# Optimization experiments

Measured on AMD Instinct MI355X. Metric: run time of the kernel, lower is better.

Reference implementation:

```python
import jax, jax.numpy as jnp
import numpy as np

B, S, H = 2, 2048, 2048
NK, NV, DK, DV = 16, 32, 128, 128
K_CONV = 4
EPS = 1e-6
KEY_DIM = NK * DK          # 2048
VALUE_DIM = NV * DV        # 4096
CONV_DIM = 2 * KEY_DIM + VALUE_DIM  # 8192
R = NV // NK               # GQA repeat factor


def setup_inputs() -> dict:
    key = jax.random.key(0)
    ks = jax.random.split(key, 9)
    s = lambda d: 1.0 / np.sqrt(d)
    x = jax.random.normal(ks[0], (B, S, H), jnp.float32)
    W_qkvz = jax.random.normal(ks[1], (H, 2 * KEY_DIM + 2 * VALUE_DIM), jnp.float32) * s(H)
    W_ba = jax.random.normal(ks[2], (H, 2 * NV), jnp.float32) * s(H)
    conv_w = jax.random.normal(ks[3], (CONV_DIM, K_CONV), jnp.float32) * s(K_CONV)
    dt_bias = jnp.ones((NV,), jnp.float32)
    A_log = jnp.log(jax.random.uniform(ks[4], (NV,), jnp.float32, 1e-3, 16.0))
    norm_w = jnp.ones((DV,), jnp.float32)
    W_out = jax.random.normal(ks[5], (VALUE_DIM, H), jnp.float32) * s(VALUE_DIM)
    return {"x": x, "W_qkvz": W_qkvz, "W_ba": W_ba, "conv_w": conv_w,
            "dt_bias": dt_bias, "A_log": A_log, "norm_w": norm_w, "W_out": W_out}


def _rms_norm(x, eps=EPS):
    return x * jax.lax.rsqrt(jnp.mean(jnp.square(x), -1, keepdims=True) + eps)


def _forward(x, W_qkvz, W_ba, conv_w, dt_bias, A_log, norm_w, W_out):
    b_, s_ = x.shape[:2]
    # in projections (mlx split-INDEX semantics)
    qkvz = (x @ W_qkvz).reshape(b_, s_, NK, 2 * DK + 2 * R * DV)
    q, k, v, z = jnp.split(qkvz, [DK, 2 * DK, 2 * DK + R * DV], axis=-1)
    v = v.reshape(b_, s_, NV, DV)
    z = z.reshape(b_, s_, NV, DV)
    ba = (x @ W_ba).reshape(b_, s_, NK, 2 * R)
    b_gate, a_gate = jnp.split(ba, [R], axis=-1)
    b_gate = b_gate.reshape(b_, s_, NV)
    a_gate = a_gate.reshape(b_, s_, NV)

    # causal depthwise conv over [q,k,v] channels, zero initial conv state
    mixed = jnp.concatenate([q.reshape(b_, s_, -1), k.reshape(b_, s_, -1),
                             v.reshape(b_, s_, -1)], axis=-1)  # [B,S,CONV_DIM]
    xc = jnp.pad(mixed, ((0, 0), (K_CONV - 1, 0), (0, 0))).transpose(0, 2, 1)  # [B,C,S+K-1]
    conv = jax.lax.conv_general_dilated(
        xc, conv_w[:, None, :], window_strides=(1,), padding='VALID',
        dimension_numbers=('NCH', 'OIH', 'NCH'), feature_group_count=CONV_DIM)
    conv = jax.nn.silu(conv).transpose(0, 2, 1)  # [B,S,CONV_DIM]
    q, k, v = jnp.split(conv, [KEY_DIM, 2 * KEY_DIM], axis=-1)
    q = q.reshape(b_, s_, NK, DK)
    k = k.reshape(b_, s_, NK, DK)
    v = v.reshape(b_, s_, NV, DV)

    inv_scale = DK ** -0.5
    q = (inv_scale ** 2) * _rms_norm(q)
    k = inv_scale * _rms_norm(k)
    # GQA: repeat k/q heads to match value heads
    q = jnp.repeat(q, R, axis=2)  # [B,S,NV,DK]
    k = jnp.repeat(k, R, axis=2)

    beta = jax.nn.sigmoid(b_gate)                                # [B,S,NV]
    g = -jnp.exp(A_log) * jax.nn.softplus(a_gate + dt_bias)      # [B,S,NV] (log-decay)

    # gated delta-rule recurrence, scan over time
    def step(Sst, inp):
        q_t, k_t, v_t, g_t, beta_t = inp   # [B,NV,DK], [B,NV,DV], [B,NV]
        Sst = Sst * jnp.exp(g_t)[..., None, None]
        kv = jnp.einsum('bhk,bhkv->bhv', k_t, Sst)
        delta = (v_t - kv) * beta_t[..., None]
        Sst = Sst + k_t[..., None] * delta[:, :, None, :]
        o = jnp.einsum('bhk,bhkv->bhv', q_t, Sst)
        return Sst, o

    S0 = jnp.zeros((b_, NV, DK, DV), x.dtype)
    xs = (q.transpose(1, 0, 2, 3), k.transpose(1, 0, 2, 3), v.transpose(1, 0, 2, 3),
          g.transpose(1, 0, 2), beta.transpose(1, 0, 2))
    _, out = jax.lax.scan(step, S0, xs)
    out = out.transpose(1, 0, 2, 3)  # [B,S,NV,DV]

    # gated RMSNorm (precise swiglu)
    xn = _rms_norm(out) * norm_w
    gated = jax.nn.silu(z.astype(jnp.float32)) * xn.astype(jnp.float32)
    gated = gated.astype(x.dtype)
    return gated.reshape(b_, s_, VALUE_DIM) @ W_out


def reference(x, W_qkvz, W_ba, conv_w, dt_bias, A_log, norm_w, W_out):
    return _forward(x, W_qkvz, W_ba, conv_w, dt_bias, A_log, norm_w, W_out)
```

## Files before the change

### kernel.cpp

```cpp
#include <hip/hip_runtime.h>
#include <stdint.h>

#define B_    2
#define SEQ   2048
#define HID   2048
#define NK_   16
#define NV_   32
#define DK_   128
#define DV_   128
#define NQKVZ 12288
#define CONVD 8192
#define MTOT  (B_*SEQ)
#define CCH   16
#define T0TOK 1216
#define HTOK2 832
#define RLDSZ 110592

typedef unsigned short ushort_t;
typedef __bf16 bf16x8 __attribute__((ext_vector_type(8)));
typedef float  f32x4  __attribute__((ext_vector_type(4)));
typedef unsigned short us4 __attribute__((ext_vector_type(4)));

__device__ __forceinline__ ushort_t f2bf(float f){
  union { float f; unsigned u; } v; v.f = f;
  unsigned r = v.u + 0x7FFFu + ((v.u >> 16) & 1u);
  return (ushort_t)(r >> 16);
}
__device__ __forceinline__ float bf2f(ushort_t u){
  union { unsigned u; float f; } v; v.u = ((unsigned)u) << 16; return v.f;
}
__device__ __forceinline__ float sigmoidf_(float x){ return 1.f/(1.f+__expf(-x)); }
__device__ __forceinline__ float siluf_(float x){ return x*sigmoidf_(x); }

__global__ void cast_x_kernel(const float* __restrict__ x, ushort_t* __restrict__ xb, int n4){
  int i = blockIdx.x*256 + threadIdx.x;
  if (i >= n4) return;
  float4 v = ((const float4*)x)[i];
  us4 o; o[0]=f2bf(v.x); o[1]=f2bf(v.y); o[2]=f2bf(v.z); o[3]=f2bf(v.w);
  ((us4*)xb)[i] = o;
}

__global__ __launch_bounds__(256) void transpose_cast(const float* __restrict__ W, ushort_t* __restrict__ Wt,
                                                      int K, int N){
  __shared__ float tile[64][65];
  int n0 = blockIdx.x*64, k0 = blockIdx.y*64;
  int tx = threadIdx.x & 63, ty = threadIdx.x >> 6;
  #pragma unroll
  for (int i=0;i<16;i++){
    int kr = ty + i*4;
    tile[kr][tx] = W[(size_t)(k0+kr)*N + n0+tx];
  }
  __syncthreads();
  #pragma unroll
  for (int i=0;i<16;i++){
    int nr = ty + i*4;
    Wt[(size_t)(n0+nr)*K + k0+tx] = f2bf(tile[tx][nr]);
  }
}

template<int OUTBF>
__global__ __launch_bounds__(512, 2) void gemm_big(const ushort_t* __restrict__ A, const ushort_t* __restrict__ Bt,
                                                   void* __restrict__ Cv, int M, int N, int K){
  extern __shared__ ushort_t dynlds[];
  ushort_t* SA = dynlds;
  ushort_t* SB = dynlds + 3*8192;
  const int t = threadIdx.x;
  const int lane = t & 63, w = t >> 6;
  const int wm = w >> 2, wn = w & 3;
  const int lr = lane & 15, hk = lane >> 4;
  const int gx = gridDim.x;
  const int nwg = gx * gridDim.y;
  const int flat = blockIdx.y*gx + blockIdx.x;
  const int cpx = nwg >> 3;
  const int swzb = (flat & 7)*cpx + (flat >> 3);
  const int m0 = (swzb / gx) * 256, n0 = (swzb % gx) * 256;

  int srow[2], scol[2];
  #pragma unroll
  for (int q=0;q<2;q++){
    int p  = (w*2+q)*1024 + lane*16;
    int lg = p ^ (((p>>9)&1)<<5);
    srow[q] = lg >> 6;
    scol[q] = (lg & 63) >> 1;
  }
  int phA[8], phB[4];
  #pragma unroll
  for (int mi=0;mi<8;mi++){
    int lg = (wm*128 + mi*16 + lr)*64 + hk*16;
    phA[mi] = lg ^ (((lg>>9)&1)<<5);
  }
  #pragma unroll
  for (int ni=0;ni<4;ni++){
    int lg = (wn*64 + ni*16 + lr)*64 + hk*16;
    phB[ni] = lg ^ (((lg>>9)&1)<<5);
  }

  auto stage = [&](int j, int bufb){
    #pragma unroll
    for (int q=0;q<2;q++)
      __builtin_amdgcn_global_load_lds(
        (const __attribute__((address_space(1))) void*)(A + (size_t)(m0+srow[q])*K + j*32 + scol[q]),
        (__attribute__((address_space(3))) void*)(SA + bufb*8192 + (w*2+q)*512), 16, 0, 0);
    #pragma unroll
    for (int q=0;q<2;q++)
      __builtin_amdgcn_global_load_lds(
        (const __attribute__((address_space(1))) void*)(Bt + (size_t)(n0+srow[q])*K + j*32 + scol[q]),
        (__attribute__((address_space(3))) void*)(SB + bufb*8192 + (w*2+q)*512), 16, 0, 0);
  };

  f32x4 acc[8][4];
  #pragma unroll
  for (int mi=0;mi<8;mi++)
    #pragma unroll
    for (int ni=0;ni<4;ni++) acc[mi][ni] = (f32x4){0.f,0.f,0.f,0.f};

  const int NT = K >> 5;
  stage(0, 0);
  stage(1, 1);
  asm volatile("s_waitcnt vmcnt(4)" ::: "memory");
  __builtin_amdgcn_s_barrier();
  __builtin_amdgcn_sched_barrier(0);

  int cur = 0;
  for (int j = 0; j < NT; ++j){
    int nb = cur + 2; if (nb >= 3) nb -= 3;
    if (j + 2 < NT) stage(j+2, nb);
    const char* bA = (const char*)(SA + cur*8192);
    const char* bB = (const char*)(SB + cur*8192);
    bf16x8 af[8], bfv[4];
    #pragma unroll
    for (int mi=0;mi<8;mi++) af[mi]  = *(const bf16x8*)(bA + phA[mi]);
    #pragma unroll
    for (int ni=0;ni<4;ni++) bfv[ni] = *(const bf16x8*)(bB + phB[ni]);
    #pragma unroll
    for (int mi=0;mi<8;mi++)
      #pragma unroll
      for (int ni=0;ni<4;ni++)
        acc[mi][ni] = __builtin_amdgcn_mfma_f32_16x16x32_bf16(af[mi], bfv[ni], acc[mi][ni], 0, 0, 0);
    if (j + 2 < NT){
      asm volatile("s_waitcnt vmcnt(4)" ::: "memory");
      __builtin_amdgcn_s_barrier();
      __builtin_amdgcn_sched_barrier(0);
    } else if (j + 1 < NT){
      asm volatile("s_waitcnt vmcnt(0)" ::: "memory");
      __builtin_amdgcn_s_barrier();
      __builtin_amdgcn_sched_barrier(0);
    }
    cur = cur + 1; if (cur >= 3) cur -= 3;
  }

  #pragma unroll
  for (int mi=0;mi<8;mi++)
    #pragma unroll
    for (int ni=0;ni<4;ni++)
      #pragma unroll
      for (int r=0;r<4;r++){
        int m = m0 + wm*128 + mi*16 + hk*4 + r;
        int n = n0 + wn*64  + ni*16 + lr;
        if (OUTBF) ((ushort_t*)Cv)[(size_t)m*N + n] = f2bf(acc[mi][ni][r]);
        else       ((float*)Cv)[(size_t)m*N + n]    = acc[mi][ni][r];
      }
}

template<int OUTBF>
__global__ __launch_bounds__(512, 2) void gemm_big2(const ushort_t* __restrict__ A, const ushort_t* __restrict__ Bt,
                                                    void* __restrict__ Cv, int M, int N, int K){
  extern __shared__ ushort_t dynlds[];
  ushort_t* SA = dynlds;
  ushort_t* SB = dynlds + 3*8192;
  const int t = threadIdx.x;
  const int lane = t & 63, w = t >> 6;
  const int wm = w >> 1, wn = w & 1;
  const int lr = lane & 15, hk = lane >> 4;
  const int gx = gridDim.x;
  const int nwg = gx * gridDim.y;
  const int flat = blockIdx.y*gx + blockIdx.x;
  const int cpx = nwg >> 3;
  const int swzb = (flat & 7)*cpx + (flat >> 3);
  const int m0 = (swzb / gx) * 256, n0 = (swzb % gx) * 128;

  int srA[2], scA[2];
  #pragma unroll
  for (int q=0;q<2;q++){
    int p  = (w*2+q)*1024 + lane*16;
    int lg = p ^ (((p>>9)&1)<<5);
    srA[q] = lg >> 6;
    scA[q] = (lg & 63) >> 1;
  }
  int srB, scB;
  {
    int p  = w*1024 + lane*16;
    int lg = p ^ (((p>>9)&1)<<5);
    srB = lg >> 6;
    scB = (lg & 63) >> 1;
  }
  int phA[4], phB[4];
  #pragma unroll
  for (int mi=0;mi<4;mi++){
    int lg = (wm*64 + mi*16 + lr)*64 + hk*16;
    phA[mi] = lg ^ (((lg>>9)&1)<<5);
  }
  #pragma unroll
  for (int ni=0;ni<4;ni++){
    int lg = (wn*64 + ni*16 + lr)*64 + hk*16;
    phB[ni] = lg ^ (((lg>>9)&1)<<5);
  }

  auto stage = [&](int j, int bufb){
    #pragma unroll
    for (int q=0;q<2;q++)
      __builtin_amdgcn_global_load_lds(
        (const __attribute__((address_space(1))) void*)(A + (size_t)(m0+srA[q])*K + j*32 + scA[q]),
        (__attribute__((address_space(3))) void*)(SA + bufb*8192 + (w*2+q)*512), 16, 0, 0);
    __builtin_amdgcn_global_load_lds(
        (const __attribute__((address_space(1))) void*)(Bt + (size_t)(n0+srB)*K + j*32 + scB),
        (__attribute__((address_space(3))) void*)(SB + bufb*4096 + w*512), 16, 0, 0);
  };

  f32x4 acc[4][4];
  #pragma unroll
  for (int mi=0;mi<4;mi++)
    #pragma unroll
    for (int ni=0;ni<4;ni++) acc[mi][ni] = (f32x4){0.f,0.f,0.f,0.f};

  const int NT = K >> 5;
  stage(0, 0);
  stage(1, 1);
  asm volatile("s_waitcnt vmcnt(3)" ::: "memory");
  __builtin_amdgcn_s_barrier();
  __builtin_amdgcn_sched_barrier(0);

  int cur = 0;
  for (int j = 0; j < NT; ++j){
    int nb = cur + 2; if (nb >= 3) nb -= 3;
    if (j + 2 < NT) stage(j+2, nb);
    const char* bA = (const char*)(SA + cur*8192);
    const char* bB = (const char*)(SB + cur*4096);
    bf16x8 af[4], bfv[4];
    #pragma unroll
    for (int mi=0;mi<4;mi++) af[mi]  = *(const bf16x8*)(bA + phA[mi]);
    #pragma unroll
    for (int ni=0;ni<4;ni++) bfv[ni] = *(const bf16x8*)(bB + phB[ni]);
    #pragma unroll
    for (int mi=0;mi<4;mi++)
      #pragma unroll
      for (int ni=0;ni<4;ni++)
        acc[mi][ni] = __builtin_amdgcn_mfma_f32_16x16x32_bf16(af[mi], bfv[ni], acc[mi][ni], 0, 0, 0);
    if (j + 2 < NT){
      asm volatile("s_waitcnt vmcnt(3)" ::: "memory");
      __builtin_amdgcn_s_barrier();
      __builtin_amdgcn_sched_barrier(0);
    } else if (j + 1 < NT){
      asm volatile("s_waitcnt vmcnt(0)" ::: "memory");
      __builtin_amdgcn_s_barrier();
      __builtin_amdgcn_sched_barrier(0);
    }
    cur = cur + 1; if (cur >= 3) cur -= 3;
  }

  #pragma unroll
  for (int mi=0;mi<4;mi++)
    #pragma unroll
    for (int ni=0;ni<4;ni++)
      #pragma unroll
      for (int r=0;r<4;r++){
        int m = m0 + wm*64 + mi*16 + hk*4 + r;
        int n = n0 + wn*64 + ni*16 + lr;
        if (OUTBF) ((ushort_t*)Cv)[(size_t)m*N + n] = f2bf(acc[mi][ni][r]);
        else       ((float*)Cv)[(size_t)m*N + n]    = acc[mi][ni][r];
      }
}

__global__ __launch_bounds__(256) void gemm_ba(const float* __restrict__ x, const float* __restrict__ Wba,
                                               float* __restrict__ ba){
  int lane = threadIdx.x & 63;
  int wid  = threadIdx.x >> 6;
  int row  = blockIdx.x*4 + wid;
  const float* xr = x + (size_t)row*HID;
  float acc = 0.f;
  for (int k=0;k<HID;k+=4){
    float4 xv = *(const float4*)&xr[k];
    acc += xv.x * Wba[(size_t)(k+0)*64 + lane];
    acc += xv.y * Wba[(size_t)(k+1)*64 + lane];
    acc += xv.z * Wba[(size_t)(k+2)*64 + lane];
    acc += xv.w * Wba[(size_t)(k+3)*64 + lane];
  }
  ba[(size_t)row*64 + lane] = acc;
}

__global__ __launch_bounds__(256) void conv_norm_kernel(const ushort_t* __restrict__ qkvz, const float* __restrict__ conv_w,
                                                        ushort_t* __restrict__ qkv){
  const int blk = blockIdx.x;
  const int bt = blk >> 4;
  const int ts = bt & (SEQ-1);
  const int gi = (blk & 15)*4 + (threadIdx.x >> 6);
  const int e2 = threadIdx.x & 63;
  const int dk = 2*e2;
  int col;
  if (gi < 16)       col = gi*768 + dk;
  else if (gi < 32)  col = (gi-16)*768 + 128 + dk;
  else { int nv = gi-32; col = (nv>>1)*768 + 256 + (nv&1)*128 + dk; }
  const int c = gi*128 + dk;
  const float4 w0 = *(const float4*)&conv_w[(size_t)c*4];
  const float4 w1 = *(const float4*)&conv_w[(size_t)(c+1)*4];
  ushort2 a0 = (ts>=3) ? *(const ushort2*)&qkvz[(size_t)(bt-3)*NQKVZ + col] : make_ushort2(0,0);
  ushort2 a1 = (ts>=2) ? *(const ushort2*)&qkvz[(size_t)(bt-2)*NQKVZ + col] : make_ushort2(0,0);
  ushort2 a2 = (ts>=1) ? *(const ushort2*)&qkvz[(size_t)(bt-1)*NQKVZ + col] : make_ushort2(0,0);
  ushort2 a3 =           *(const ushort2*)&qkvz[(size_t)(bt  )*NQKVZ + col];
  float y0 = siluf_(bf2f(a0.x)*w0.x + bf2f(a1.x)*w0.y + bf2f(a2.x)*w0.z + bf2f(a3.x)*w0.w);
  float y1 = siluf_(bf2f(a0.y)*w1.x + bf2f(a1.y)*w1.y + bf2f(a2.y)*w1.z + bf2f(a3.y)*w1.w);
  float o0 = y0, o1 = y1;
  if (gi < 32){
    float ss = y0*y0 + y1*y1;
    #pragma unroll
    for (int o=1;o<64;o<<=1) ss += __shfl_xor(ss, o);
    float rs = rsqrtf(ss*(1.f/128.f) + 1e-6f);
    float scale = (gi < 16) ? (1.f/128.f) : 0.08838834764831845f;
    o0 = y0*rs*scale; o1 = y1*rs*scale;
  }
  ushort2 ov; ov.x = f2bf(o0); ov.y = f2bf(o1);
  *(ushort2*)&qkv[(size_t)bt*CONVD + gi*128 + dk] = ov;
}

__global__ void gbeta_kernel(const float* __restrict__ ba, const float* __restrict__ A_log,
                             const float* __restrict__ dt_bias, float2* __restrict__ egb){
  int idx = blockIdx.x*256 + threadIdx.x;
  if (idx >= MTOT*NV_) return;
  int nv = idx & 31;
  int bt = idx >> 5;
  int nk = nv >> 1, r = nv & 1;
  float bg = ba[(size_t)bt*64 + nk*4 + r];
  float ag = ba[(size_t)bt*64 + nk*4 + 2 + r];
  float ad = ag + dt_bias[nv];
  float sp = fmaxf(ad, 0.f) + log1pf(__expf(-fabsf(ad)));
  float g  = -__expf(A_log[nv]) * sp;
  egb[idx] = make_float2(g, sigmoidf_(bg));
}

__global__ __launch_bounds__(512) void recurrence_chunked(const ushort_t* __restrict__ qkv,
                                                          const float2* __restrict__ egb,
                                                          float* __restrict__ outc,
                                                          ushort_t* __restrict__ oaug,
                                                          ushort_t* __restrict__ Sfin,
                                                          int pmode){
  extern __shared__ char rlds[];
  ushort_t* Kl  = (ushort_t*)(rlds + 0);
  ushort_t* S0h = (ushort_t*)(rlds + 4352);
  ushort_t* S0l = (ushort_t*)(rlds + 21760);
  ushort_t* T0h = (ushort_t*)(rlds + 39168);
  ushort_t* T0l = (ushort_t*)(rlds + 56576);
  ushort_t* KT  = (ushort_t*)(rlds + 73984);
  ushort_t* DT  = (ushort_t*)(rlds + 84224);
  ushort_t* Wl  = (ushort_t*)(rlds + 94464);
  float*    Al  = (float*)   (rlds + 95744);
  float*    Ul  = (float*)   (rlds + 97024);
  float*    clB = (float*)   (rlds + 107264);
  float*    blB = clB + 32;
  float*    eclB= clB + 64;
  float*    kslB= clB + 96;
  float*    c15B= clB + 128;

  const int bi = blockIdx.x;
  int hb, tokbase, ntok;
  bool ismrg = false, wsf = false;
  if (pmode == 0){ hb = bi; tokbase = 0; ntok = SEQ; }
  else {
    if (bi < 128){ hb = bi; tokbase = 0; ntok = T0TOK; wsf = true; }
    else { hb = bi - 128; tokbase = T0TOK; ntok = HTOK2; ismrg = true; }
  }
  const int b    = hb >> 6;
  const int nv   = (hb >> 1) & 31;
  const int half = hb & 1;
  const int nk   = nv >> 1;
  const int t    = threadIdx.x;
  const int lane = t & 63, w = t >> 6;
  const int lr   = lane & 15, hk = lane >> 4;

  for (int i = t; i < 128*40; i += 512){ KT[i] = 0; DT[i] = 0; }
  for (int i = t; i < 16*40;  i += 512) Wl[i] = 0;
  for (int i = t; i < 64*136; i += 512){
    S0h[i] = 0; S0l[i] = 0;
    if (ismrg){ T0h[i] = 0; T0l[i] = 0; }
  }
  __syncthreads();
  if (ismrg && t < 64) T0h[t*136 + half*64 + t] = (ushort_t)0x3F80;

  const int dt  = w >> 1;
  const int dkb = (w & 1) * 4;
  const int ot  = w - 4;
  const int st  = t >> 5, sdk = (t & 31) * 4;
  const size_t bt0 = (size_t)b*SEQ + tokbase;
  const int mytile = (w < 4) ? w : (w - 4);

  f32x4 S[4], T[4];
  #pragma unroll
  for (int tt=0;tt<4;tt++)
    #pragma unroll
    for (int r=0;r<4;r++){
      S[tt][r] = 0.f;
      T[tt][r] = (ismrg && ((dkb+tt)*16 + hk*4 + r) == (half*64 + dt*16 + lr)) ? 1.f : 0.f;
    }

  uint2 kreg = *(const uint2*)(qkv + (bt0+st)*CONVD + 2048 + nk*128 + sdk);
  bf16x8 qf[4];
  if (w >= 4){
    const ushort_t* qrow = qkv + (bt0+lr)*CONVD + nk*128 + hk*8;
    #pragma unroll
    for (int ks=0;ks<4;ks++) qf[ks] = *(const bf16x8*)(qrow + ks*32);
  }
  ushort_t vreg[4] = {0,0,0,0};
  if (w < 4){
    #pragma unroll
    for (int r=0;r<4;r++)
      vreg[r] = qkv[(bt0+hk*4+r)*CONVD + 4096 + nv*128 + half*64 + w*16 + lr];
  }
  {
    float2 gb = make_float2(0.f,0.f);
    if (w==1 && lane<16) gb = egb[(bt0+lane)*NV_ + nv];
    *(uint2*)&Kl[st*136 + sdk] = kreg;
    if (w==1 && lane<16){
      float c = gb.x;
      #pragma unroll
      for (int o=1;o<16;o<<=1){ float tv = __shfl_up(c, o, 16); if (lane >= o) c += tv; }
      clB[lane] = c; blB[lane] = gb.y; eclB[lane] = __expf(c);
      float c15 = __shfl(c, 15, 16);
      kslB[lane] = __expf(c15 - c);
      if (lane==0) c15B[0] = c15;
    }
  }
  __syncthreads();

  int pb = 0;
  for (int base = 0; base < ntok; base += CCH){
    const int nbase = (base + CCH < ntok) ? base + CCH : base;
    const int pb16 = pb*16;

    bf16x8 kf[4];
    if (w <= 4){
      #pragma unroll
      for (int ks=0;ks<4;ks++) kf[ks] = *(const bf16x8*)&Kl[lr*136 + hk*8 + ks*32];
    }
    f32x4 ph = (f32x4){0.f,0.f,0.f,0.f}, pl = ph, phA = ph, plA = ph;
    __builtin_amdgcn_s_setprio(1);
    #pragma unroll
    for (int ks=0;ks<4;ks++){
      bf16x8 xf = (w < 4) ? kf[ks] : qf[ks];
      bf16x8 yh = *(const bf16x8*)&S0h[(mytile*16+lr)*136 + hk*8 + ks*32];
      bf16x8 yl = *(const bf16x8*)&S0l[(mytile*16+lr)*136 + hk*8 + ks*32];
      ph = __builtin_amdgcn_mfma_f32_16x16x32_bf16(xf, yh, ph, 0,0,0);
      pl = __builtin_amdgcn_mfma_f32_16x16x32_bf16(xf, yl, pl, 0,0,0);
    }
    if (ismrg){
      #pragma unroll
      for (int ks=0;ks<4;ks++){
        bf16x8 xf = (w < 4) ? kf[ks] : qf[ks];
        bf16x8 yh = *(const bf16x8*)&T0h[(mytile*16+lr)*136 + hk*8 + ks*32];
        bf16x8 yl = *(const bf16x8*)&T0l[(mytile*16+lr)*136 + hk*8 + ks*32];
        phA = __builtin_amdgcn_mfma_f32_16x16x32_bf16(xf, yh, phA, 0,0,0);
        plA = __builtin_amdgcn_mfma_f32_16x16x32_bf16(xf, yl, plA, 0,0,0);
      }
    }
    __builtin_amdgcn_s_setprio(0);
    if (w == 1){
      f32x4 a = (f32x4){0.f,0.f,0.f,0.f};
      #pragma unroll
      for (int ks=0;ks<4;ks++) a = __builtin_amdgcn_mfma_f32_16x16x32_bf16(kf[ks], kf[ks], a, 0,0,0);
      #pragma unroll
      for (int r=0;r<4;r++){
        int i = hk*4 + r, j = lr;
        Al[i*20 + j] = (j < i) ? blB[pb16+i]*__expf(clB[pb16+i]-clB[pb16+j])*a[r] : 0.f;
      }
    }
    if (w == 4){
      f32x4 a = (f32x4){0.f,0.f,0.f,0.f};
      #pragma unroll
      for (int ks=0;ks<4;ks++) a = __builtin_amdgcn_mfma_f32_16x16x32_bf16(qf[ks], kf[ks], a, 0,0,0);
      #pragma unroll
      for (int r=0;r<4;r++){
        int i = hk*4 + r, j = lr;
        float val = (j <= i) ? __expf(clB[pb16+i]-clB[pb16+j])*a[r] : 0.f;
        Wl[i*40 + j] = f2bf(val);
      }
    }
    if (w < 4){
      float4 uu;
      #pragma unroll
      for (int r=0;r<4;r++){
        int i = hk*4 + r;
        ((float*)&uu)[r] = blB[pb16+i]*(bf2f(vreg[r]) - eclB[pb16+i]*(ph[r] + pl[r]));
      }
      *(float4*)&Ul[(w*16 + lr)*20 + hk*4] = uu;
      if (ismrg){
        float4 ua;
        #pragma unroll
        for (int r=0;r<4;r++){
          int i = hk*4 + r;
          ((float*)&ua)[r] = -blB[pb16+i]*eclB[pb16+i]*(phA[r] + plA[r]);
        }
        *(float4*)&Ul[(64 + w*16 + lr)*20 + hk*4] = ua;
      }
    }
    if (w == 2 || w == 3){
      int dk = t & 127;
      #pragma unroll
      for (int j=0;j<16;j+=2){
        unsigned p0 = f2bf(kslB[pb16+j]  * bf2f(Kl[j*136     + dk]));
        unsigned p1 = f2bf(kslB[pb16+j+1]* bf2f(Kl[(j+1)*136 + dk]));
        *(unsigned*)&KT[dk*40 + j] = p0 | (p1 << 16);
      }
    }
    __syncthreads();

    kreg = *(const uint2*)(qkv + (bt0+nbase+st)*CONVD + 2048 + nk*128 + sdk);
    if (w >= 4){
      const ushort_t* qrow = qkv + (bt0 + nbase + lr)*CONVD + nk*128 + hk*8;
      #pragma unroll
      for (int ks=0;ks<4;ks++) qf[ks] = *(const bf16x8*)(qrow + ks*32);
    }
    if (w < 4){
      #pragma unroll
      for (int r=0;r<4;r++)
        vreg[r] = qkv[(bt0+nbase+hk*4+r)*CONVD + 4096 + nv*128 + half*64 + w*16 + lr];
    }
    float2 ebn = make_float2(0.f,0.f);
    if (w==1 && lane<16) ebn = egb[(bt0+nbase+lane)*NV_ + nv];
    bf16x8 yf[4];
    #pragma unroll
    for (int tt=0;tt<4;tt++) yf[tt] = *(const bf16x8*)&KT[((dkb+tt)*16+lr)*40 + hk*8];
    bf16x8 wfr;
    if (w >= 4) wfr = *(const bf16x8*)&Wl[lr*40 + hk*8];

    auto fsub = [&](int rowoff){
      float d[16];
      #pragma unroll
      for (int q=0;q<4;q++){
        float4 dd = *(const float4*)&Ul[(rowoff+lane)*20 + q*4];
        d[4*q]=dd.x; d[4*q+1]=dd.y; d[4*q+2]=dd.z; d[4*q+3]=dd.w;
      }
      #pragma unroll
      for (int rb=0;rb<4;rb++){
        float p0=0.f,p1=0.f,p2=0.f,p3=0.f;
        #pragma unroll
        for (int jb=0;jb<rb;jb++){
          float4 A0 = *(const float4*)&Al[(rb*4+0)*20 + jb*4];
          float4 A1 = *(const float4*)&Al[(rb*4+1)*20 + jb*4];
          float4 A2 = *(const float4*)&Al[(rb*4+2)*20 + jb*4];
          float4 A3 = *(const float4*)&Al[(rb*4+3)*20 + jb*4];
          p0 += A0.x*d[jb*4]+A0.y*d[jb*4+1]+A0.z*d[jb*4+2]+A0.w*d[jb*4+3];
          p1 += A1.x*d[jb*4]+A1.y*d[jb*4+1]+A1.z*d[jb*4+2]+A1.w*d[jb*4+3];
          p2 += A2.x*d[jb*4]+A2.y*d[jb*4+1]+A2.z*d[jb*4+2]+A2.w*d[jb*4+3];
          p3 += A3.x*d[jb*4]+A3.y*d[jb*4+1]+A3.z*d[jb*4+2]+A3.w*d[jb*4+3];
        }
        const int r0 = rb*4;
        d[r0+0] -= p0;
        d[r0+1] -= p1 + Al[(r0+1)*20+r0]*d[r0];
        d[r0+2] -= p2 + Al[(r0+2)*20+r0]*d[r0] + Al[(r0+2)*20+r0+1]*d[r0+1];
        d[r0+3] -= p3 + Al[(r0+3)*20+r0]*d[r0] + Al[(r0+3)*20+r0+1]*d[r0+1] + Al[(r0+3)*20+r0+2]*d[r0+2];
      }
      unsigned dd[8];
      #pragma unroll
      for (int p=0;p<8;p++) dd[p] = (unsigned)f2bf(d[2*p]) | ((unsigned)f2bf(d[2*p+1]) << 16);
      *(uint4*)&DT[(rowoff+lane)*40 + 0] = make_uint4(dd[0],dd[1],dd[2],dd[3]);
      *(uint4*)&DT[(rowoff+lane)*40 + 8] = make_uint4(dd[4],dd[5],dd[6],dd[7]);
    };
    if (w == 0){ __builtin_amdgcn_s_setprio(1); fsub(0);  __builtin_amdgcn_s_setprio(0); }
    if (ismrg && w == 1){ __builtin_amdgcn_s_setprio(1); fsub(64); __builtin_amdgcn_s_setprio(0); }
    __syncthreads();

    if (w >= 4){
      bf16x8 dfr = *(const bf16x8*)&DT[(ot*16+lr)*40 + hk*8];
      f32x4 oo = __builtin_amdgcn_mfma_f32_16x16x32_bf16(wfr, dfr, (f32x4){0.f,0.f,0.f,0.f}, 0,0,0);
      #pragma unroll
      for (int r=0;r<4;r++){
        int i = hk*4 + r;
        outc[((bt0+base+i)*NV_ + nv)*(size_t)DV_ + half*64 + ot*16 + lr] = oo[r] + eclB[pb16+i]*(ph[r] + pl[r]);
      }
      if (ismrg){
        bf16x8 dfr2 = *(const bf16x8*)&DT[(64 + ot*16+lr)*40 + hk*8];
        f32x4 oo2 = __builtin_amdgcn_mfma_f32_16x16x32_bf16(wfr, dfr2, (f32x4){0.f,0.f,0.f,0.f}, 0,0,0);
        #pragma unroll
        for (int r=0;r<4;r++){
          int i = hk*4 + r;
          oaug[(((size_t)(b*NV_+nv))*HTOK2 + base + i)*128 + half*64 + ot*16 + lr]
            = f2bf(oo2[r] + eclB[pb16+i]*(phA[r] + plA[r]));
        }
      }
    }
    {
      float g15 = __expf(c15B[pb]);
      bf16x8 dB = *(const bf16x8*)&DT[(dt*16+lr)*40 + hk*8];
      __builtin_amdgcn_s_setprio(1);
      #pragma unroll
      for (int tt=0;tt<4;tt++){
        f32x4 s = S[tt];
        s[0]*=g15; s[1]*=g15; s[2]*=g15; s[3]*=g15;
        S[tt] = __builtin_amdgcn_mfma_f32_16x16x32_bf16(yf[tt], dB, s, 0,0,0);
      }
      if (ismrg){
        bf16x8 dB2 = *(const bf16x8*)&DT[(64 + dt*16+lr)*40 + hk*8];
        #pragma unroll
        for (int tt=0;tt<4;tt++){
          f32x4 s = T[tt];
          s[0]*=g15; s[1]*=g15; s[2]*=g15; s[3]*=g15;
          T[tt] = __builtin_amdgcn_mfma_f32_16x16x32_bf16(yf[tt], dB2, s, 0,0,0);
        }
      }
      __builtin_amdgcn_s_setprio(0);
    }
    {
      const int dv = dt*16 + lr;
      #pragma unroll
      for (int tt=0;tt<4;tt++){
        const int dk0 = (dkb+tt)*16 + hk*4;
        {
          float s0=S[tt][0], s1=S[tt][1], s2=S[tt][2], s3=S[tt][3];
          ushort_t h0=f2bf(s0), h1=f2bf(s1), h2=f2bf(s2), h3=f2bf(s3);
          *(uint2*)&S0h[dv*136 + dk0] = make_uint2((unsigned)h0 | ((unsigned)h1<<16),
                                                   (unsigned)h2 | ((unsigned)h3<<16));
          *(uint2*)&S0l[dv*136 + dk0] = make_uint2((unsigned)f2bf(s0-bf2f(h0)) | ((unsigned)f2bf(s1-bf2f(h1))<<16),
                                                   (unsigned)f2bf(s2-bf2f(h2)) | ((unsigned)f2bf(s3-bf2f(h3))<<16));
        }
        if (ismrg){
          float s0=T[tt][0], s1=T[tt][1], s2=T[tt][2], s3=T[tt][3];
          ushort_t h0=f2bf(s0), h1=f2bf(s1), h2=f2bf(s2), h3=f2bf(s3);
          *(uint2*)&T0h[dv*136 + dk0] = make_uint2((unsigned)h0 | ((unsigned)h1<<16),
                                                   (unsigned)h2 | ((unsigned)h3<<16));
          *(uint2*)&T0l[dv*136 + dk0] = make_uint2((unsigned)f2bf(s0-bf2f(h0)) | ((unsigned)f2bf(s1-bf2f(h1))<<16),
                                                   (unsigned)f2bf(s2-bf2f(h2)) | ((unsigned)f2bf(s3-bf2f(h3))<<16));
        }
      }
    }
    *(uint2*)&Kl[st*136 + sdk] = kreg;
    if (w==1 && lane<16){
      float c = ebn.x;
      #pragma unroll
      for (int o=1;o<16;o<<=1){ float tv = __shfl_up(c, o, 16); if (lane >= o) c += tv; }
      int q16 = (pb^1)*16;
      clB[q16+lane] = c; blB[q16+lane] = ebn.y; eclB[q16+lane] = __expf(c);
      float c15 = __shfl(c, 15, 16);
      kslB[q16+lane] = __expf(c15 - c);
      if (lane==0) c15B[pb^1] = c15;
    }
    __syncthreads();
    pb ^= 1;
  }

  if (wsf){
    for (int i = t; i < 64*128; i += 512){
      int dvl = i >> 7, dk = i & 127;
      size_t row = ((size_t)(b*NV_+nv)*128 + half*64 + dvl)*256;
      Sfin[row + dk]       = S0h[dvl*136 + dk];
      Sfin[row + 128 + dk] = S0l[dvl*136 + dk];
    }
  }
}

__global__ __launch_bounds__(256) void corr_gemm(const ushort_t* __restrict__ oaug, const ushort_t* __restrict__ Sfin,
                                                 float* __restrict__ core){
  __shared__ ushort_t As[128][32];
  __shared__ ushort_t Bs[128][32];
  const int head = blockIdx.y;
  const int m0 = blockIdx.x * 128;
  const int b = head >> 5, nv = head & 31;
  const int t = threadIdx.x, lane = t & 63, w = t >> 6;
  const int wm = w >> 1, wn = w & 1;
  const int srow = lane >> 2, scol = (lane & 3) * 8;
  const ushort_t* Abase = oaug + (size_t)head*HTOK2*128;
  const ushort_t* Bbase = Sfin + (size_t)head*128*256;
  ushort_t* lA0 = &As[     w*16][0];
  ushort_t* lA1 = &As[64 + w*16][0];
  ushort_t* lB0 = &Bs[     w*16][0];
  ushort_t* lB1 = &Bs[64 + w*16][0];
  f32x4 acc[4][4];
  #pragma unroll
  for (int i=0;i<4;i++)
    #pragma unroll
    for (int j=0;j<4;j++) acc[i][j] = (f32x4){0.f,0.f,0.f,0.f};
  const int lr = lane & 15, lk = (lane >> 4) * 8;
  for (int k0 = 0; k0 < 256; k0 += 32){
    const int ka = k0 & 127;
    __builtin_amdgcn_global_load_lds((const __attribute__((address_space(1))) void*)(Abase + (size_t)(m0 +      w*16 + srow)*128 + ka + scol),
                                     (__attribute__((address_space(3))) void*)lA0, 16, 0, 0);
    __builtin_amdgcn_global_load_lds((const __attribute__((address_space(1))) void*)(Abase + (size_t)(m0 + 64 + w*16 + srow)*128 + ka + scol),
                                     (__attribute__((address_space(3))) void*)lA1, 16, 0, 0);
    __builtin_amdgcn_global_load_lds((const __attribute__((address_space(1))) void*)(Bbase + (size_t)(     w*16 + srow)*256 + k0 + scol),
                                     (__attribute__((address_space(3))) void*)lB0, 16, 0, 0);
    __builtin_amdgcn_global_load_lds((const __attribute__((address_space(1))) void*)(Bbase + (size_t)(64 + w*16 + srow)*256 + k0 + scol),
                                     (__attribute__((address_space(3))) void*)lB1, 16, 0, 0);
    __syncthreads();
    bf16x8 af[4], bfv[4];
    #pragma unroll
    for (int i=0;i<4;i++) af[i]  = *(const bf16x8*)&As[wm*64 + i*16 + lr][lk];
    #pragma unroll
    for (int j=0;j<4;j++) bfv[j] = *(const bf16x8*)&Bs[wn*64 + j*16 + lr][lk];
    #pragma unroll
    for (int i=0;i<4;i++)
      #pragma unroll
      for (int j=0;j<4;j++)
        acc[i][j] = __builtin_amdgcn_mfma_f32_16x16x32_bf16(af[i], bfv[j], acc[i][j], 0, 0, 0);
    __syncthreads();
  }
  const int lg = lane >> 4;
  #pragma unroll
  for (int i=0;i<4;i++)
    #pragma unroll
    for (int j=0;j<4;j++)
      #pragma unroll
      for (int r=0;r<4;r++){
        int m = m0 + wm*64 + i*16 + lg*4 + r;
        int n = wn*64 + j*16 + lr;
        if (m < HTOK2){
          float* p = &core[(((size_t)b*SEQ + T0TOK + m)*NV_ + nv)*(size_t)DV_ + n];
          *p += acc[i][j][r];
        }
      }
}

__global__ __launch_bounds__(128) void gatenorm_kernel(const float* __restrict__ outc, const ushort_t* __restrict__ qkvz,
                                                       const float* __restrict__ norm_w, ushort_t* __restrict__ gated){
  __shared__ float red[2];
  const int blk = blockIdx.x;
  const int nv = blk & 31;
  const size_t bt = (size_t)(blk >> 5);
  const int dv = threadIdx.x;
  float xv = outc[(bt*NV_ + nv)*(size_t)DV_ + dv];
  float ss = xv*xv;
  #pragma unroll
  for (int o=1;o<64;o<<=1) ss += __shfl_xor(ss, o);
  if ((threadIdx.x & 63)==0) red[threadIdx.x>>6] = ss;
  __syncthreads();
  float tot = red[0]+red[1];
  float xn = xv * rsqrtf(tot*(1.f/128.f) + 1e-6f) * norm_w[dv];
  int nk = nv>>1, r = nv&1;
  float z = bf2f(qkvz[bt*NQKVZ + nk*768 + 512 + r*128 + dv]);
  gated[bt*(size_t)4096 + nv*128 + dv] = f2bf(siluf_(z)*xn);
}

extern "C" void kernel_launch(void* const* d_in, const int* in_sizes, int n_in,
                              void* d_out, int out_size, void* d_ws, size_t ws_size,
                              hipStream_t stream){
  (void)in_sizes; (void)n_in; (void)out_size;
  const float* x      = (const float*)d_in[0];
  const float* W_qkvz = (const float*)d_in[1];
  const float* W_ba   = (const float*)d_in[2];
  const float* conv_w = (const float*)d_in[3];
  const float* dt_bias= (const float*)d_in[4];
  const float* A_log  = (const float*)d_in[5];
  const float* norm_w = (const float*)d_in[6];
  const float* W_out  = (const float*)d_in[7];
  float* outp = (float*)d_out;

  char* w = (char*)d_ws;
  const size_t R0 = 0;
  const size_t R1 = 100663296;
  const size_t R2 = R1 + 67108864;
  const size_t R3 = R2 + 67108864;
  const size_t R4 = R3 + 2097152;
  const size_t NEED_SP = R4 + 16777216 + 4194304;
  ushort_t* qkvz_bf = (ushort_t*)(w + R0);
  ushort_t* xb      = (ushort_t*)(w + R1);
  ushort_t* wqt     = (ushort_t*)(w + R1 + 16777216);
  ushort_t* qkv_bf  = (ushort_t*)(w + R1);
  ushort_t* gated   = (ushort_t*)(w + R1);
  float*    core    = (float*)   (w + R2);
  ushort_t* wot     = (ushort_t*)(w + R2);
  float*    ba      = (float*)   (w + R3);
  float2*   egb     = (float2*)  (w + R3 + 1048576);
  ushort_t* oaug    = (ushort_t*)(w + R4);
  ushort_t* Sfin    = (ushort_t*)(w + R4 + 16777216);

  hipError_t e1 = hipFuncSetAttribute((const void*)gemm_big<1>, hipFuncAttributeMaxDynamicSharedMemorySize, 98304);
  hipError_t e2 = hipFuncSetAttribute((const void*)gemm_big2<0>, hipFuncAttributeMaxDynamicSharedMemorySize, 73728);
  hipError_t e3 = hipFuncSetAttribute((const void*)recurrence_chunked, hipFuncAttributeMaxDynamicSharedMemorySize, RLDSZ);
  (void)e1; (void)e2;
  const bool seqpar = (ws_size >= NEED_SP) && (e3 == hipSuccess);

  cast_x_kernel<<<(MTOT*HID/4 + 255)/256, 256, 0, stream>>>(x, xb, MTOT*HID/4);
  transpose_cast<<<dim3(NQKVZ/64, HID/64), 256, 0, stream>>>(W_qkvz, wqt, HID, NQKVZ);
  gemm_big<1><<<dim3(NQKVZ/256, MTOT/256), 512, 98304, stream>>>(xb, wqt, (void*)qkvz_bf, MTOT, NQKVZ, HID);
  gemm_ba<<<MTOT/4, 256, 0, stream>>>(x, W_ba, ba);
  gbeta_kernel<<<(MTOT*NV_+255)/256, 256, 0, stream>>>(ba, A_log, dt_bias, egb);
  conv_norm_kernel<<<MTOT*16, 256, 0, stream>>>(qkvz_bf, conv_w, qkv_bf);
  if (seqpar){
    recurrence_chunked<<<256, 512, RLDSZ, stream>>>(qkv_bf, egb, core, oaug, Sfin, 1);
    corr_gemm<<<dim3((HTOK2 + 127)/128, 64), 256, 0, stream>>>(oaug, Sfin, core);
  } else {
    recurrence_chunked<<<128, 512, RLDSZ, stream>>>(qkv_bf, egb, core, oaug, Sfin, 0);
  }
  gatenorm_kernel<<<MTOT*NV_, 128, 0, stream>>>(core, qkvz_bf, norm_w, gated);
  transpose_cast<<<dim3(2048/64, 4096/64), 256, 0, stream>>>(W_out, wot, 4096, 2048);
  gemm_big2<0><<<dim3(2048/128, MTOT/256), 512, 73728, stream>>>(gated, wot, (void*)outp, MTOT, 2048, 4096);
}
```

Baseline: 874.5 us.

## Process 8 tokens per conv block with sliding window and rebalance sequence split

The conv+norm kernel now handles CT=8 consecutive tokens per block, keeping a sliding window of the previous three inputs in registers instead of reloading four rows per token, and launches 8x fewer blocks. Separately, the sequence-parallel split point moves (T0TOK/HTOK2 changed) to rebalance the two halves of the chunked recurrence, and corr_gemm row loads are clamped because HTOK2 is no longer a multiple of 128. The aim is to cut redundant global loads and launch overhead in the conv stage and to shorten the critical path of the recurrence. Fewer blocks mean less parallelism, and the new split must line up with chunk boundaries inside the recurrence.

```diff
diff --git a/kernel.cpp b/kernel.cpp
--- a/kernel.cpp
+++ b/kernel.cpp
@@ -12,8 +12,9 @@
 #define CONVD 8192
 #define MTOT  (B_*SEQ)
 #define CCH   16
-#define T0TOK 1216
-#define HTOK2 832
+#define T0TOK 1264
+#define HTOK2 784
+#define CT    8
 #define RLDSZ 110592
 
 typedef unsigned short ushort_t;
@@ -291,8 +292,8 @@
 __global__ __launch_bounds__(256) void conv_norm_kernel(const ushort_t* __restrict__ qkvz, const float* __restrict__ conv_w,
                                                         ushort_t* __restrict__ qkv){
   const int blk = blockIdx.x;
-  const int bt = blk >> 4;
-  const int ts = bt & (SEQ-1);
+  const int bt0 = (blk >> 4) * CT;
+  const int ts0 = bt0 & (SEQ-1);
   const int gi = (blk & 15)*4 + (threadIdx.x >> 6);
   const int e2 = threadIdx.x & 63;
   const int dk = 2*e2;
@@ -303,23 +304,28 @@
   const int c = gi*128 + dk;
   const float4 w0 = *(const float4*)&conv_w[(size_t)c*4];
   const float4 w1 = *(const float4*)&conv_w[(size_t)(c+1)*4];
-  ushort2 a0 = (ts>=3) ? *(const ushort2*)&qkvz[(size_t)(bt-3)*NQKVZ + col] : make_ushort2(0,0);
-  ushort2 a1 = (ts>=2) ? *(const ushort2*)&qkvz[(size_t)(bt-2)*NQKVZ + col] : make_ushort2(0,0);
-  ushort2 a2 = (ts>=1) ? *(const ushort2*)&qkvz[(size_t)(bt-1)*NQKVZ + col] : make_ushort2(0,0);
-  ushort2 a3 =           *(const ushort2*)&qkvz[(size_t)(bt  )*NQKVZ + col];
-  float y0 = siluf_(bf2f(a0.x)*w0.x + bf2f(a1.x)*w0.y + bf2f(a2.x)*w0.z + bf2f(a3.x)*w0.w);
-  float y1 = siluf_(bf2f(a0.y)*w1.x + bf2f(a1.y)*w1.y + bf2f(a2.y)*w1.z + bf2f(a3.y)*w1.w);
-  float o0 = y0, o1 = y1;
-  if (gi < 32){
-    float ss = y0*y0 + y1*y1;
-    #pragma unroll
-    for (int o=1;o<64;o<<=1) ss += __shfl_xor(ss, o);
-    float rs = rsqrtf(ss*(1.f/128.f) + 1e-6f);
-    float scale = (gi < 16) ? (1.f/128.f) : 0.08838834764831845f;
-    o0 = y0*rs*scale; o1 = y1*rs*scale;
-  }
-  ushort2 ov; ov.x = f2bf(o0); ov.y = f2bf(o1);
-  *(ushort2*)&qkv[(size_t)bt*CONVD + gi*128 + dk] = ov;
+  ushort2 h0 = (ts0>=1) ? *(const ushort2*)&qkvz[(size_t)(bt0-3)*NQKVZ + col] : make_ushort2(0,0);
+  ushort2 h1 = (ts0>=1) ? *(const ushort2*)&qkvz[(size_t)(bt0-2)*NQKVZ + col] : make_ushort2(0,0);
+  ushort2 h2 = (ts0>=1) ? *(const ushort2*)&qkvz[(size_t)(bt0-1)*NQKVZ + col] : make_ushort2(0,0);
+  const float scale = (gi < 16) ? (1.f/128.f) : 0.08838834764831845f;
+  #pragma unroll
+  for (int tt=0; tt<CT; ++tt){
+    const int bt = bt0 + tt;
+    ushort2 h3 = *(const ushort2*)&qkvz[(size_t)bt*NQKVZ + col];
+    float y0 = siluf_(bf2f(h0.x)*w0.x + bf2f(h1.x)*w0.y + bf2f(h2.x)*w0.z + bf2f(h3.x)*w0.w);
+    float y1 = siluf_(bf2f(h0.y)*w1.x + bf2f(h1.y)*w1.y + bf2f(h2.y)*w1.z + bf2f(h3.y)*w1.w);
+    float o0 = y0, o1 = y1;
+    if (gi < 32){
+      float ss = y0*y0 + y1*y1;
+      #pragma unroll
+      for (int o=1;o<64;o<<=1) ss += __shfl_xor(ss, o);
+      float rs = rsqrtf(ss*(1.f/128.f) + 1e-6f);
+      o0 = y0*rs*scale; o1 = y1*rs*scale;
+    }
+    ushort2 ov; ov.x = f2bf(o0); ov.y = f2bf(o1);
+    *(ushort2*)&qkv[(size_t)bt*CONVD + gi*128 + dk] = ov;
+    h0 = h1; h1 = h2; h2 = h3;
+  }
 }
 
 __global__ void gbeta_kernel(const float* __restrict__ ba, const float* __restrict__ A_log,
@@ -679,9 +685,11 @@
   const int lr = lane & 15, lk = (lane >> 4) * 8;
   for (int k0 = 0; k0 < 256; k0 += 32){
     const int ka = k0 & 127;
-    __builtin_amdgcn_global_load_lds((const __attribute__((address_space(1))) void*)(Abase + (size_t)(m0 +      w*16 + srow)*128 + ka + scol),
+    int ra0 = m0 +      w*16 + srow; if (ra0 >= HTOK2) ra0 = HTOK2 - 1;
+    int ra1 = m0 + 64 + w*16 + srow; if (ra1 >= HTOK2) ra1 = HTOK2 - 1;
+    __builtin_amdgcn_global_load_lds((const __attribute__((address_space(1))) void*)(Abase + (size_t)ra0*128 + ka + scol),
                                      (__attribute__((address_space(3))) void*)lA0, 16, 0, 0);
-    __builtin_amdgcn_global_load_lds((const __attribute__((address_space(1))) void*)(Abase + (size_t)(m0 + 64 + w*16 + srow)*128 + ka + scol),
+    __builtin_amdgcn_global_load_lds((const __attribute__((address_space(1))) void*)(Abase + (size_t)ra1*128 + ka + scol),
                                      (__attribute__((address_space(3))) void*)lA1, 16, 0, 0);
     __builtin_amdgcn_global_load_lds((const __attribute__((address_space(1))) void*)(Bbase + (size_t)(     w*16 + srow)*256 + k0 + scol),
                                      (__attribute__((address_space(3))) void*)lB0, 16, 0, 0);
@@ -780,7 +788,7 @@
   gemm_big<1><<<dim3(NQKVZ/256, MTOT/256), 512, 98304, stream>>>(xb, wqt, (void*)qkvz_bf, MTOT, NQKVZ, HID);
   gemm_ba<<<MTOT/4, 256, 0, stream>>>(x, W_ba, ba);
   gbeta_kernel<<<(MTOT*NV_+255)/256, 256, 0, stream>>>(ba, A_log, dt_bias, egb);
-  conv_norm_kernel<<<MTOT*16, 256, 0, stream>>>(qkvz_bf, conv_w, qkv_bf);
+  conv_norm_kernel<<<(MTOT/CT)*16, 256, 0, stream>>>(qkvz_bf, conv_w, qkv_bf);
   if (seqpar){
     recurrence_chunked<<<256, 512, RLDSZ, stream>>>(qkv_bf, egb, core, oaug, Sfin, 1);
     corr_gemm<<<dim3((HTOK2 + 127)/128, 64), 256, 0, stream>>>(oaug, Sfin, core);
```

Measured after the change: 853.1 us. 2.4% less time.
